# Optimization experiments

Measured on AMD Instinct MI355X. Metric: run time of the kernel, lower is better.

Reference implementation:

```python
import jax, jax.numpy as jnp
import numpy as np

B, S, E2, E = 2, 512, 512, 256  # batch, seq, 2*encode_size, encode_size


def setup_inputs() -> dict:
    key = jax.random.key(0)
    k1, k2, k3, k4 = jax.random.split(key, 4)
    query = jax.random.normal(k1, (B, S, E2), dtype=jnp.float32)
    value = jax.random.normal(k2, (B, S, E2), dtype=jnp.float32)
    # nn.Linear weights (no bias); stored as [in, out] for x @ W convention
    Wd = jax.random.normal(k3, (E2, E), dtype=jnp.float32) * (1.0 / np.sqrt(E2))
    vd = jax.random.normal(k4, (E,), dtype=jnp.float32) * (1.0 / np.sqrt(E))
    return {"query": query, "value": value, "Wd": Wd, "vd": vd}


def reference(query, value, Wd, vd):
    # q = query.unsqueeze(1) -> [B,1,S,2E]; k = query.unsqueeze(2) -> [B,S,1,2E]
    # NOTE: original module ignores its `key` arg; both factors come from query.
    qk = query[:, None, :, :] * query[:, :, None, :]        # [B,S,S,2E]
    h = jnp.tanh(jnp.einsum('bsth,hd->bstd', qk, Wd))        # [B,S,S,E]
    sjt = jnp.einsum('bstd,d->bst', h, vd)                   # [B,S,S]
    atten = jax.nn.softmax(sjt, axis=2)                      # softmax over dim=2
    # dropout p=0.0 -> identity
    context = jnp.einsum('bst,btd->bsd', atten, value)       # bmm
    return (context, atten)
```

## Files before the change

kernel.cpp:

```cpp
#include <hip/hip_runtime.h>

#define B_  2
#define S_  512
#define E2_ 512
#define E_  256

#define TT  64
#define KB  32
#define KS  64
#define LDK 72

using f32x4 = __attribute__((ext_vector_type(4))) float;
using f16x8 = __attribute__((ext_vector_type(8))) _Float16;

__device__ __forceinline__ float tanh_fast(float x) {
    float e = __expf(2.0f * x);
    return 1.0f - 2.0f / (e + 1.0f);
}

__global__ void prep_all(const float* __restrict__ q, _Float16* __restrict__ qh,
                         const float* __restrict__ Wd, _Float16* __restrict__ Wp2) {
    int idx = blockIdx.x * 256 + threadIdx.x;
    float4 v = *(const float4*)(q + idx * 4);
    _Float16 h4[4] = {(_Float16)v.x, (_Float16)v.y, (_Float16)v.z, (_Float16)v.w};
    *(short4*)(qh + idx * 4) = *(short4*)h4;
    int h = idx >> 8;
    int d = idx & 255;
    int ko = h >> 5;
    int kk = h & 31;
    Wp2[ko * (E_ * KB) + d * KB + kk] = (_Float16)Wd[idx];
}

__global__ __launch_bounds__(256, 4)
void stage1(const _Float16* __restrict__ qh,
            const _Float16* __restrict__ Wp2,
            const float* __restrict__ vd,
            float* __restrict__ logits ) {
    const int x  = blockIdx.x;
    const int p  = x >> 6;
    const int sl = x & 63;
    const int b  = blockIdx.y;
    int sj = 0;
    while ((sj + 1) * (sj + 2) / 2 <= p) ++sj;
    const int ti = p - sj * (sj + 1) / 2;
    const int s  = sj * TT + sl;
    const int t0 = ti * TT;

    __shared__ _Float16 sA[2][TT * LDK];
    __shared__ _Float16 sQsh[E2_];
    __shared__ float sVd[E_];

    const int tid = threadIdx.x;
    {
        const _Float16* qsrow = qh + ((size_t)(b * S_ + s)) * E2_;
        sQsh[tid]       = qsrow[tid];
        sQsh[tid + 256] = qsrow[tid + 256];
        sVd[tid & 255]  = vd[tid & 255];
    }
    __syncthreads();

    const int wave = tid >> 6;
    const int lane = tid & 63;
    const int wd   = wave;
    const int l15  = lane & 15;
    const int l4   = lane >> 4;

    const int a_row = tid >> 2;
    const int a_g   = tid & 3;
    const int a_off = a_row * LDK + a_g * 16;
    const _Float16* qt = qh + ((size_t)(b * S_ + t0 + a_row)) * E2_ + a_g * 16;

    const _Float16* wpb = Wp2 + (wd * 64 + l15) * KB + l4 * 8;

    f16x8 ra0, ra1;
    auto ALOAD = [&](int j) {
        ra0 = *(const f16x8*)(qt + j * KS);
        ra1 = *(const f16x8*)(qt + j * KS + 8);
    };
    auto AWRITE = [&](int hh) {
        *(f16x8*)&sA[hh][a_off]     = ra0;
        *(f16x8*)&sA[hh][a_off + 8] = ra1;
    };

    f32x4 acc[4][4] = {};

    ALOAD(0);
    AWRITE(0);
    ALOAD(1);
    asm volatile("s_waitcnt lgkmcnt(0)" ::: "memory");
    __builtin_amdgcn_s_barrier();

    for (int ko = 0; ko < 8; ++ko) {
        const int h  = ko & 1;
        const int k0 = ko * KS;
        f16x8 bf[4], af[4], qsv, pa[4];

        {
            const _Float16* wk = wpb + (2 * ko) * (E_ * KB);
#pragma unroll
            for (int fd = 0; fd < 4; ++fd)
                bf[fd] = *(const f16x8*)(wk + fd * 16 * KB);
        }
#pragma unroll
        for (int ft = 0; ft < 4; ++ft) {
            int row = ft * 16 + l15;
            af[ft] = *(const f16x8*)&sA[h][row * LDK + l4 * 8];
        }
        qsv = *(const f16x8*)&sQsh[k0 + l4 * 8];
#pragma unroll
        for (int ft = 0; ft < 4; ++ft) pa[ft] = af[ft] * qsv;
        __builtin_amdgcn_s_setprio(1);
#pragma unroll
        for (int ft = 0; ft < 4; ++ft)
#pragma unroll
            for (int fd = 0; fd < 4; ++fd)
                acc[ft][fd] = __builtin_amdgcn_mfma_f32_16x16x32_f16(pa[ft], bf[fd], acc[ft][fd], 0, 0, 0);
        __builtin_amdgcn_s_setprio(0);

        {
            const _Float16* wk = wpb + (2 * ko + 1) * (E_ * KB);
#pragma unroll
            for (int fd = 0; fd < 4; ++fd)
                bf[fd] = *(const f16x8*)(wk + fd * 16 * KB);
        }
#pragma unroll
        for (int ft = 0; ft < 4; ++ft) {
            int row = ft * 16 + l15;
            af[ft] = *(const f16x8*)&sA[h][row * LDK + 32 + l4 * 8];
        }
        qsv = *(const f16x8*)&sQsh[k0 + 32 + l4 * 8];
        if (ko < 7) AWRITE(h ^ 1);
        if (ko < 6) ALOAD(ko + 2);
#pragma unroll
        for (int ft = 0; ft < 4; ++ft) pa[ft] = af[ft] * qsv;
        __builtin_amdgcn_s_setprio(1);
#pragma unroll
        for (int ft = 0; ft < 4; ++ft)
#pragma unroll
            for (int fd = 0; fd < 4; ++fd)
                acc[ft][fd] = __builtin_amdgcn_mfma_f32_16x16x32_f16(pa[ft], bf[fd], acc[ft][fd], 0, 0, 0);
        __builtin_amdgcn_s_setprio(0);
        if (ko < 7) {
            asm volatile("s_waitcnt lgkmcnt(0)" ::: "memory");
            __builtin_amdgcn_s_barrier();
        }
    }

    __syncthreads();

    float* sRed = (float*)&sA[0][0];
    {
        float vdr[4];
#pragma unroll
        for (int fd = 0; fd < 4; ++fd) vdr[fd] = sVd[wd * 64 + fd * 16 + l15];
#pragma unroll
        for (int ft = 0; ft < 4; ++ft) {
#pragma unroll
            for (int r = 0; r < 4; ++r) {
                float pp = 0.f;
#pragma unroll
                for (int fd = 0; fd < 4; ++fd)
                    pp += tanh_fast(acc[ft][fd][r]) * vdr[fd];
                pp += __shfl_xor(pp, 1);
                pp += __shfl_xor(pp, 2);
                pp += __shfl_xor(pp, 4);
                pp += __shfl_xor(pp, 8);
                if (l15 == 0) {
                    int tl = ft * 16 + l4 * 4 + r;
                    sRed[tl * 4 + wd] = pp;
                }
            }
        }
    }
    __syncthreads();
    if (tid < TT) {
        float v = sRed[tid * 4 + 0] + sRed[tid * 4 + 1] + sRed[tid * 4 + 2] + sRed[tid * 4 + 3];
        int t = t0 + tid;
        logits[((size_t)(b * S_ + s)) * S_ + t] = v;
        logits[((size_t)(b * S_ + t)) * S_ + s] = v;
    }
}

__global__ void softmax_k(float* __restrict__ atten) {
    const int row  = blockIdx.x;
    const int lane = threadIdx.x;
    float* p = atten + (size_t)row * S_;
    float4 v0 = *(float4*)(p + lane * 8);
    float4 v1 = *(float4*)(p + lane * 8 + 4);
    float vv[8] = {v0.x, v0.y, v0.z, v0.w, v1.x, v1.y, v1.z, v1.w};
    float m = vv[0];
#pragma unroll
    for (int j = 1; j < 8; ++j) m = fmaxf(m, vv[j]);
#pragma unroll
    for (int off = 1; off < 64; off <<= 1) m = fmaxf(m, __shfl_xor(m, off));
    float ssum = 0.f;
#pragma unroll
    for (int j = 0; j < 8; ++j) { vv[j] = __expf(vv[j] - m); ssum += vv[j]; }
#pragma unroll
    for (int off = 1; off < 64; off <<= 1) ssum += __shfl_xor(ssum, off);
    float inv = 1.0f / ssum;
    float4 o0 = {vv[0] * inv, vv[1] * inv, vv[2] * inv, vv[3] * inv};
    float4 o1 = {vv[4] * inv, vv[5] * inv, vv[6] * inv, vv[7] * inv};
    *(float4*)(p + lane * 8)     = o0;
    *(float4*)(p + lane * 8 + 4) = o1;
}

__global__ __launch_bounds__(256)
void context_k(const float* __restrict__ atten, const float* __restrict__ value,
               float* __restrict__ ctx) {
    __shared__ float sA[32][65];
    __shared__ float sV[64][65];
    const int b  = blockIdx.z;
    const int s0 = blockIdx.y * 32;
    const int e0 = blockIdx.x * 64;
    const int tid = threadIdx.x;
    const int ts = tid >> 4;
    const int te = tid & 15;

    float acc[2][4] = {};
    for (int k0 = 0; k0 < S_; k0 += 64) {
        {
            int r = tid >> 3;
            int c = (tid & 7) * 8;
            const float* ga = atten + ((size_t)(b * S_ + s0 + r)) * S_ + k0 + c;
            *(float4*)&sA[r][c]     = *(const float4*)ga;
            *(float4*)&sA[r][c + 4] = *(const float4*)(ga + 4);
        }
        {
            int r = tid >> 2;
            int c = (tid & 3) * 16;
            const float* gv = value + ((size_t)(b * S_ + k0 + r)) * E2_ + e0 + c;
#pragma unroll
            for (int j = 0; j < 16; j += 4)
                *(float4*)&sV[r][c + j] = *(const float4*)(gv + j);
        }
        __syncthreads();
#pragma unroll 8
        for (int kk = 0; kk < 64; ++kk) {
            float a0 = sA[ts * 2 + 0][kk];
            float a1 = sA[ts * 2 + 1][kk];
#pragma unroll
            for (int j = 0; j < 4; ++j) {
                float vvv = sV[kk][te * 4 + j];
                acc[0][j] += a0 * vvv;
                acc[1][j] += a1 * vvv;
            }
        }
        __syncthreads();
    }
#pragma unroll
    for (int i = 0; i < 2; ++i)
#pragma unroll
        for (int j = 0; j < 4; ++j)
            ctx[((size_t)(b * S_ + s0 + ts * 2 + i)) * E2_ + e0 + te * 4 + j] = acc[i][j];
}

extern "C" void kernel_launch(void* const* d_in, const int* in_sizes, int n_in,
                              void* d_out, int out_size, void* d_ws, size_t ws_size,
                              hipStream_t stream) {
    const float* query = (const float*)d_in[0];
    const float* value = (const float*)d_in[1];
    const float* Wd    = (const float*)d_in[2];
    const float* vd    = (const float*)d_in[3];

    float* out   = (float*)d_out;
    float* ctx   = out;
    float* atten = out + (size_t)B_ * S_ * E2_;

    const size_t need = (size_t)(B_ * S_ * E2_ + 16 * E_ * KB) * sizeof(_Float16);
    _Float16* qh;
    if (ws_size >= need) {
        qh = (_Float16*)d_ws;
    } else {
        qh = (_Float16*)ctx;
    }
    _Float16* wp2 = qh + (size_t)B_ * S_ * E2_;

    prep_all<<<dim3(512), dim3(256), 0, stream>>>(query, qh, Wd, wp2);
    stage1<<<dim3(2304, B_), dim3(256), 0, stream>>>(qh, wp2, vd, atten);
    softmax_k<<<dim3(B_ * S_), dim3(64), 0, stream>>>(atten);
    context_k<<<dim3(E2_ / 64, S_ / 32, B_), dim3(256), 0, stream>>>(atten, value, ctx);
}
```

Measured before the change: 143.7 us.

## Use a 2x2 wave tiling and fold the query-row scaling into the shared-memory A write

Waves now split the 64x256 output tile as 2 (t) x 2 (d), each owning a 32x128 sub-tile instead of 64x64. That changes the ratio of A reads from LDS to B reads from global/L2. The per-fragment multiply by the shared query row moves out of the MFMA inner loop into the staging write, so each element is scaled once per block instead of once per wave. The cost is more B-fragment loads per wave and a changed reduction layout.

```diff
diff --git a/kernel.cpp b/kernel.cpp
--- a/kernel.cpp
+++ b/kernel.cpp
@@ -61,7 +61,8 @@
 
     const int wave = tid >> 6;
     const int lane = tid & 63;
-    const int wd   = wave;
+    const int wt   = wave >> 1;
+    const int wd   = wave & 1;
     const int l15  = lane & 15;
     const int l4   = lane >> 4;
 
@@ -70,76 +71,65 @@
     const int a_off = a_row * LDK + a_g * 16;
     const _Float16* qt = qh + ((size_t)(b * S_ + t0 + a_row)) * E2_ + a_g * 16;
 
-    const _Float16* wpb = Wp2 + (wd * 64 + l15) * KB + l4 * 8;
+    const _Float16* wpb = Wp2 + (wd * 128 + l15) * KB + l4 * 8;
 
     f16x8 ra0, ra1;
     auto ALOAD = [&](int j) {
         ra0 = *(const f16x8*)(qt + j * KS);
         ra1 = *(const f16x8*)(qt + j * KS + 8);
     };
-    auto AWRITE = [&](int hh) {
-        *(f16x8*)&sA[hh][a_off]     = ra0;
-        *(f16x8*)&sA[hh][a_off + 8] = ra1;
+    auto AWRITE = [&](int j, int hh) {
+        f16x8 q0 = *(const f16x8*)&sQsh[j * KS + a_g * 16];
+        f16x8 q1 = *(const f16x8*)&sQsh[j * KS + a_g * 16 + 8];
+        *(f16x8*)&sA[hh][a_off]     = ra0 * q0;
+        *(f16x8*)&sA[hh][a_off + 8] = ra1 * q1;
     };
 
-    f32x4 acc[4][4] = {};
+    f32x4 acc[2][8] = {};
 
     ALOAD(0);
-    AWRITE(0);
+    AWRITE(0, 0);
     ALOAD(1);
     asm volatile("s_waitcnt lgkmcnt(0)" ::: "memory");
     __builtin_amdgcn_s_barrier();
 
     for (int ko = 0; ko < 8; ++ko) {
-        const int h  = ko & 1;
-        const int k0 = ko * KS;
-        f16x8 bf[4], af[4], qsv, pa[4];
-
-        {
-            const _Float16* wk = wpb + (2 * ko) * (E_ * KB);
+        const int h = ko & 1;
+        f16x8 af[2], bf[4];
+
+#pragma unroll
+        for (int hx = 0; hx < 2; ++hx) {
+            const _Float16* wk = wpb + (2 * ko + hx) * (E_ * KB);
+#pragma unroll
+            for (int ft = 0; ft < 2; ++ft) {
+                int row = wt * 32 + ft * 16 + l15;
+                af[ft] = *(const f16x8*)&sA[h][row * LDK + hx * 32 + l4 * 8];
+            }
+            if (hx == 1) {
+                if (ko < 7) AWRITE(ko + 1, h ^ 1);
+                if (ko < 6) ALOAD(ko + 2);
+            }
 #pragma unroll
             for (int fd = 0; fd < 4; ++fd)
                 bf[fd] = *(const f16x8*)(wk + fd * 16 * KB);
-        }
-#pragma unroll
-        for (int ft = 0; ft < 4; ++ft) {
-            int row = ft * 16 + l15;
-            af[ft] = *(const f16x8*)&sA[h][row * LDK + l4 * 8];
-        }
-        qsv = *(const f16x8*)&sQsh[k0 + l4 * 8];
-#pragma unroll
-        for (int ft = 0; ft < 4; ++ft) pa[ft] = af[ft] * qsv;
-        __builtin_amdgcn_s_setprio(1);
-#pragma unroll
-        for (int ft = 0; ft < 4; ++ft)
+            __builtin_amdgcn_s_setprio(1);
+#pragma unroll
+            for (int ft = 0; ft < 2; ++ft)
+#pragma unroll
+                for (int fd = 0; fd < 4; ++fd)
+                    acc[ft][fd] = __builtin_amdgcn_mfma_f32_16x16x32_f16(af[ft], bf[fd], acc[ft][fd], 0, 0, 0);
+            __builtin_amdgcn_s_setprio(0);
 #pragma unroll
             for (int fd = 0; fd < 4; ++fd)
-                acc[ft][fd] = __builtin_amdgcn_mfma_f32_16x16x32_f16(pa[ft], bf[fd], acc[ft][fd], 0, 0, 0);
-        __builtin_amdgcn_s_setprio(0);
-
-        {
-            const _Float16* wk = wpb + (2 * ko + 1) * (E_ * KB);
-#pragma unroll
-            for (int fd = 0; fd < 4; ++fd)
-                bf[fd] = *(const f16x8*)(wk + fd * 16 * KB);
-        }
-#pragma unroll
-        for (int ft = 0; ft < 4; ++ft) {
-            int row = ft * 16 + l15;
-            af[ft] = *(const f16x8*)&sA[h][row * LDK + 32 + l4 * 8];
-        }
-        qsv = *(const f16x8*)&sQsh[k0 + 32 + l4 * 8];
-        if (ko < 7) AWRITE(h ^ 1);
-        if (ko < 6) ALOAD(ko + 2);
-#pragma unroll
-        for (int ft = 0; ft < 4; ++ft) pa[ft] = af[ft] * qsv;
-        __builtin_amdgcn_s_setprio(1);
-#pragma unroll
-        for (int ft = 0; ft < 4; ++ft)
-#pragma unroll
-            for (int fd = 0; fd < 4; ++fd)
-                acc[ft][fd] = __builtin_amdgcn_mfma_f32_16x16x32_f16(pa[ft], bf[fd], acc[ft][fd], 0, 0, 0);
-        __builtin_amdgcn_s_setprio(0);
+                bf[fd] = *(const f16x8*)(wk + (fd + 4) * 16 * KB);
+            __builtin_amdgcn_s_setprio(1);
+#pragma unroll
+            for (int ft = 0; ft < 2; ++ft)
+#pragma unroll
+                for (int fd = 0; fd < 4; ++fd)
+                    acc[ft][fd + 4] = __builtin_amdgcn_mfma_f32_16x16x32_f16(af[ft], bf[fd], acc[ft][fd + 4], 0, 0, 0);
+            __builtin_amdgcn_s_setprio(0);
+        }
         if (ko < 7) {
             asm volatile("s_waitcnt lgkmcnt(0)" ::: "memory");
             __builtin_amdgcn_s_barrier();
@@ -150,31 +140,31 @@
 
     float* sRed = (float*)&sA[0][0];
     {
-        float vdr[4];
-#pragma unroll
-        for (int fd = 0; fd < 4; ++fd) vdr[fd] = sVd[wd * 64 + fd * 16 + l15];
-#pragma unroll
-        for (int ft = 0; ft < 4; ++ft) {
+        float vdr[8];
+#pragma unroll
+        for (int fd = 0; fd < 8; ++fd) vdr[fd] = sVd[wd * 128 + fd * 16 + l15];
+#pragma unroll
+        for (int ft = 0; ft < 2; ++ft) {
 #pragma unroll
             for (int r = 0; r < 4; ++r) {
                 float pp = 0.f;
 #pragma unroll
-                for (int fd = 0; fd < 4; ++fd)
+                for (int fd = 0; fd < 8; ++fd)
                     pp += tanh_fast(acc[ft][fd][r]) * vdr[fd];
                 pp += __shfl_xor(pp, 1);
                 pp += __shfl_xor(pp, 2);
                 pp += __shfl_xor(pp, 4);
                 pp += __shfl_xor(pp, 8);
                 if (l15 == 0) {
-                    int tl = ft * 16 + l4 * 4 + r;
-                    sRed[tl * 4 + wd] = pp;
+                    int tl = wt * 32 + ft * 16 + l4 * 4 + r;
+                    sRed[tl * 2 + wd] = pp;
                 }
             }
         }
     }
     __syncthreads();
     if (tid < TT) {
-        float v = sRed[tid * 4 + 0] + sRed[tid * 4 + 1] + sRed[tid * 4 + 2] + sRed[tid * 4 + 3];
+        float v = sRed[tid * 2 + 0] + sRed[tid * 2 + 1];
         int t = t0 + tid;
         logits[((size_t)(b * S_ + s)) * S_ + t] = v;
         logits[((size_t)(b * S_ + t)) * S_ + s] = v;
```

Result: slower. 193.4 us (+34.6%).
